# Kernel optimization log

Hardware: AMD Instinct MI355X
Metric: run time of the kernel (lower is better)

The kernel has to match this reference:

```python
import jax, jax.numpy as jnp
import numpy as np

DIM = 1024      # dim
FW = 14         # focal_window
FL = 2          # focal_level
FF = 4          # focal_factor


def _dwconv_gelu(x, w, b):
    # x: [B, C, S], w: [C, 1, k] depthwise kernel, torch 'same' padding
    k = w.shape[-1]
    y = jax.lax.conv_general_dilated(
        x, w, window_strides=(1,), padding=[((k - 1) // 2, k // 2)],
        feature_group_count=x.shape[1], dimension_numbers=('NCH', 'OIH', 'NCH'))
    return jax.nn.gelu(y + b[None, :, None], approximate=False)


def setup_inputs() -> dict:
    key = jax.random.key(0)
    ks = jax.random.split(key, 8)
    B, S, D = 8, 4096, DIM
    P = 2 * D + FL + 1  # 2051
    s = 0.02
    return {
        'input': jax.random.normal(ks[0], (B, S, D), jnp.float32),
        'W_in': jax.random.normal(ks[1], (D, P), jnp.float32) * s,
        'b_in': jnp.zeros((P,), jnp.float32),
        'w0': jax.random.normal(ks[2], (D, 1, FW), jnp.float32) * s,
        'b0': jnp.zeros((D,), jnp.float32),
        'w1': jax.random.normal(ks[3], (D, 1, FF + FW), jnp.float32) * s,  # kernel 18
        'b1': jnp.zeros((D,), jnp.float32),
        'W_ctx': jax.random.normal(ks[4], (D, D), jnp.float32) * s,
        'b_ctx': jnp.zeros((D,), jnp.float32),
        'W_out': jax.random.normal(ks[5], (D, D), jnp.float32) * s,
        'b_out': jnp.zeros((D,), jnp.float32),
    }


def reference(input, W_in, b_in, w0, b0, w1, b1, W_ctx, b_ctx, W_out, b_out):
    D = DIM
    # in_proj then permute to channel-first [B, 2D+FL+1, S]
    proj = (input @ W_in + b_in).transpose(0, 2, 1)
    query = proj[:, :D]            # [B, D, S]
    ctx = proj[:, D:2 * D]         # [B, D, S]
    gates = proj[:, 2 * D:]        # [B, FL+1, S]
    # hierarchical depthwise conv pyramid (context fed through successive levels)
    c0 = _dwconv_gelu(ctx, w0, b0)
    c1 = _dwconv_gelu(c0, w1, b1)
    context_all = c0 * gates[:, 0:1] + c1 * gates[:, 1:2]
    # global context branch
    g = jax.nn.gelu(c1.mean(axis=-1), approximate=False)  # [B, D]
    context_all = context_all + g[..., None] * gates[:, FL:FL + 1]
    # context_proj is a 1x1 conv == per-position linear over channels
    modulator = jnp.einsum('oc,bcs->bos', W_ctx, context_all) + b_ctx[None, :, None]
    out = (query * modulator).transpose(0, 2, 1)  # [B, S, D]
    return out @ W_out + b_out
```

## Files before the change

### kernel.cpp

```cpp
#include <hip/hip_runtime.h>

#define DIMC 1024
#define BATCH 8
#define SEQ 4096
#define BS (BATCH*SEQ)
#define PCOL 2051

typedef unsigned short ushort_t;
typedef __attribute__((ext_vector_type(8))) short short8;
typedef __attribute__((ext_vector_type(4))) float f32x4;
typedef __attribute__((ext_vector_type(4))) unsigned short us4;

__device__ __forceinline__ float bf2f(ushort_t u) {
    union { unsigned u32; float f; } v; v.u32 = ((unsigned)u) << 16; return v.f;
}
__device__ __forceinline__ ushort_t f2bf(float f) {
    union { float f; unsigned u; } v; v.f = f;
    unsigned r = v.u + 0x7fffu + ((v.u >> 16) & 1u);
    return (ushort_t)(r >> 16);
}
__device__ __forceinline__ float gelu_exact(float x) {
    return 0.5f * x * (1.0f + erff(x * 0.7071067811865475f));
}
__device__ __forceinline__ void gld16(const ushort_t* g, ushort_t* l) {
    __builtin_amdgcn_global_load_lds(
        (const __attribute__((address_space(1))) unsigned int*)g,
        (__attribute__((address_space(3))) unsigned int*)l, 16, 0, 0);
}

__global__ void cvt_f32_bf16(const float* __restrict__ src, ushort_t* __restrict__ dst, int n) {
    int i = (blockIdx.x * 256 + threadIdx.x) * 4;
    if (i >= n) return;
    f32x4 v = *(const f32x4*)(src + i);
    us4 o;
    #pragma unroll
    for (int j = 0; j < 4; j++) o[j] = f2bf(v[j]);
    *(us4*)(dst + i) = o;
}

__global__ void transpose_cvt(const float* __restrict__ src, ushort_t* __restrict__ dst,
                              int ld, int K) {
    __shared__ float tile[32][33];
    int tx = threadIdx.x & 31, ty = threadIdx.x >> 5;
    int n0 = blockIdx.x * 32, k0 = blockIdx.y * 32;
    #pragma unroll
    for (int j = 0; j < 4; j++)
        tile[ty + j * 8][tx] = src[(size_t)(k0 + ty + j * 8) * ld + n0 + tx];
    __syncthreads();
    #pragma unroll
    for (int j = 0; j < 4; j++)
        dst[(size_t)(n0 + ty + j * 8) * K + k0 + tx] = f2bf(tile[tx][ty + j * 8]);
}

__global__ void pack_gatesw(const float* __restrict__ W_in, float* __restrict__ wg) {
    int d = blockIdx.x * 256 + threadIdx.x;
    if (d >= 1024) return;
    const float* p = W_in + (size_t)d * PCOL + 2048;
    wg[d] = p[0]; wg[1024 + d] = p[1]; wg[2048 + d] = p[2];
}

__global__ void cvt_gates(const float* __restrict__ input, const float* __restrict__ wg,
                          const float* __restrict__ b_in, ushort_t* __restrict__ ibf,
                          float* __restrict__ gates) {
    int row = blockIdx.x, tid = threadIdx.x;
    int lane = tid & 63, wave = tid >> 6;
    size_t base = (size_t)row * 1024 + tid * 4;
    f32x4 v = *(const f32x4*)(input + base);
    us4 o;
    #pragma unroll
    for (int j = 0; j < 4; j++) o[j] = f2bf(v[j]);
    *(us4*)(ibf + base) = o;
    f32x4 w0v = *(const f32x4*)(wg + tid * 4);
    f32x4 w1v = *(const f32x4*)(wg + 1024 + tid * 4);
    f32x4 w2v = *(const f32x4*)(wg + 2048 + tid * 4);
    float a0 = 0, a1 = 0, a2 = 0;
    #pragma unroll
    for (int j = 0; j < 4; j++) { a0 += v[j] * w0v[j]; a1 += v[j] * w1v[j]; a2 += v[j] * w2v[j]; }
    #pragma unroll
    for (int off = 32; off; off >>= 1) {
        a0 += __shfl_down(a0, off, 64);
        a1 += __shfl_down(a1, off, 64);
        a2 += __shfl_down(a2, off, 64);
    }
    __shared__ float red[4][3];
    if (lane == 0) { red[wave][0] = a0; red[wave][1] = a1; red[wave][2] = a2; }
    __syncthreads();
    if (tid == 0) {
        gates[row * 4 + 0] = red[0][0] + red[1][0] + red[2][0] + red[3][0] + b_in[2048];
        gates[row * 4 + 1] = red[0][1] + red[1][1] + red[2][1] + red[3][1] + b_in[2049];
        gates[row * 4 + 2] = red[0][2] + red[1][2] + red[2][2] + red[3][2] + b_in[2050];
    }
}

template<int MODE>
__global__ __launch_bounds__(512, 2)
void gemm256(const ushort_t* __restrict__ A, const ushort_t* __restrict__ Bt,
             const float* __restrict__ bias, void* __restrict__ C,
             const ushort_t* __restrict__ Q, const float* __restrict__ gates,
             const float* __restrict__ vb, int K, int ldc, int ldq, int nbx, int tpb) {
    __shared__ ushort_t lA[2][16384];
    __shared__ ushort_t lB[2][16384];
    const int tid = threadIdx.x, lane = tid & 63, wave = tid >> 6;
    const int lr = lane & 15, kq = lane >> 4;
    const int wrm = wave >> 2, wrn = wave & 3;

    const int bid = blockIdx.x;
    const int chunk = (gridDim.x >> 3) * tpb;
    const int tile0 = (bid & 7) * chunk + (bid >> 3) * tpb;

    const int xsw = kq ^ (((lr >> 3) & 1) << 1);
    const int fBase = lr * 32 + xsw * 8;

    int srOff[2][2], ldsC[2][2];
    #pragma unroll
    for (int h = 0; h < 2; h++)
        #pragma unroll
        for (int j = 0; j < 2; j++) {
            int c = h * 1024 + j * 512 + tid;
            int sub = c >> 6, rl = (c >> 2) & 15, cc = c & 3;
            int r  = ((sub >> 1) << 4) | rl;
            int k8 = ((sub & 1) << 2) | (cc ^ (((rl >> 3) & 1) << 1));
            srOff[h][j] = r * K + k8 * 8;
            ldsC[h][j]  = (h * 1024 + j * 512 + (wave << 6)) << 3;
        }

    f32x4 acc[8][4];
    short8 af[2][2], bfr[4][2];

#define STG(ARR, bb, G, kt, h) do { \
    gld16((G) + (size_t)(kt) * 64 + srOff[h][0], &ARR[bb][ldsC[h][0]]); \
    gld16((G) + (size_t)(kt) * 64 + srOff[h][1], &ARR[bb][ldsC[h][1]]); \
} while (0)

#define PHASE(bb, qq, STAGE_STMT, DOVM) do { \
    if ((qq) == 0) { \
        _Pragma("unroll") \
        for (int nt = 0; nt < 4; nt++) { \
            bfr[nt][0] = *(const short8*)&lB[bb][fBase + ((wrn * 4 + nt) * 2 + 0) * 512]; \
            bfr[nt][1] = *(const short8*)&lB[bb][fBase + ((wrn * 4 + nt) * 2 + 1) * 512]; \
        } \
    } \
    af[0][0] = *(const short8*)&lA[bb][fBase + ((wrm * 8 + (qq) * 2 + 0) * 2 + 0) * 512]; \
    af[0][1] = *(const short8*)&lA[bb][fBase + ((wrm * 8 + (qq) * 2 + 0) * 2 + 1) * 512]; \
    af[1][0] = *(const short8*)&lA[bb][fBase + ((wrm * 8 + (qq) * 2 + 1) * 2 + 0) * 512]; \
    af[1][1] = *(const short8*)&lA[bb][fBase + ((wrm * 8 + (qq) * 2 + 1) * 2 + 1) * 512]; \
    STAGE_STMT; \
    __builtin_amdgcn_s_barrier(); \
    asm volatile("s_waitcnt lgkmcnt(0)" ::: "memory"); \
    __builtin_amdgcn_s_setprio(1); \
    _Pragma("unroll") \
    for (int mi = 0; mi < 2; mi++) \
        _Pragma("unroll") \
        for (int nt = 0; nt < 4; nt++) { \
            acc[(qq) * 2 + mi][nt] = __builtin_amdgcn_mfma_f32_16x16x32_bf16( \
                af[mi][0], bfr[nt][0], acc[(qq) * 2 + mi][nt], 0, 0, 0); \
            acc[(qq) * 2 + mi][nt] = __builtin_amdgcn_mfma_f32_16x16x32_bf16( \
                af[mi][1], bfr[nt][1], acc[(qq) * 2 + mi][nt], 0, 0, 0); \
        } \
    __builtin_amdgcn_s_setprio(0); \
    if (DOVM) asm volatile("s_waitcnt vmcnt(4)" ::: "memory"); \
    __builtin_amdgcn_s_barrier(); \
} while (0)

    const int KT = K >> 6;
    const int IT = K >> 7;

    int j = tile0;
    int bn = j % nbx, bm = j / nbx;
    const ushort_t* Ag = A + (size_t)bm * 256 * K;
    const ushort_t* Bg = Bt + (size_t)bn * 256 * K;

    STG(lA, 0, Ag, 0, 0); STG(lA, 0, Ag, 0, 1);
    STG(lB, 0, Bg, 0, 0); STG(lB, 0, Bg, 0, 1);
    STG(lB, 1, Bg, 1, 0); STG(lB, 1, Bg, 1, 1);
    asm volatile("s_waitcnt vmcnt(4)" ::: "memory");
    __builtin_amdgcn_s_barrier();

    for (int ti = 0; ti < tpb; ti++) {
        const int jn = (ti < tpb - 1) ? j + 1 : j;
        const int bnn = jn % nbx, bmn = jn / nbx;
        const ushort_t* Agn = A + (size_t)bmn * 256 * K;
        const ushort_t* Bgn = Bt + (size_t)bnn * 256 * K;

        #pragma unroll
        for (int i = 0; i < 8; i++)
            #pragma unroll
            for (int jj = 0; jj < 4; jj++)
                #pragma unroll
                for (int r = 0; r < 4; r++) acc[i][jj][r] = 0.f;

        for (int it = 0; it < IT - 1; it++) {
            const int t1 = 2 * it + 1, t2 = 2 * it + 2, t3 = 2 * it + 3;
            PHASE(0, 0, STG(lA, 1, Ag, t1, 0), 0);
            PHASE(0, 1, STG(lA, 1, Ag, t1, 1); STG(lB, 0, Bg, t2, 0), 0);
            PHASE(0, 2, STG(lB, 0, Bg, t2, 1), 0);
            PHASE(0, 3, (void)0, 1);
            PHASE(1, 0, STG(lA, 0, Ag, t2, 0), 0);
            PHASE(1, 1, STG(lA, 0, Ag, t2, 1); STG(lB, 1, Bg, t3, 0), 0);
            PHASE(1, 2, STG(lB, 1, Bg, t3, 1), 0);
            PHASE(1, 3, (void)0, 1);
        }
        PHASE(0, 0, STG(lA, 1, Ag, KT - 1, 0), 0);
        PHASE(0, 1, STG(lA, 1, Ag, KT - 1, 1); STG(lB, 0, Bgn, 0, 0), 0);
        PHASE(0, 2, STG(lB, 0, Bgn, 0, 1), 0);
        PHASE(0, 3, (void)0, 1);
        PHASE(1, 0, STG(lA, 0, Agn, 0, 0), 0);
        PHASE(1, 1, STG(lA, 0, Agn, 0, 1); STG(lB, 1, Bgn, 1, 0), 0);
        PHASE(1, 2, STG(lB, 1, Bgn, 1, 1), 0);
        PHASE(1, 3, (void)0, 1);

        const int bbatch = (bm * 256) >> 12;
        float biasv[4], vbv[4];
        #pragma unroll
        for (int nt = 0; nt < 4; nt++) {
            int col = bn * 256 + wrn * 64 + nt * 16 + lr;
            biasv[nt] = bias[col];
            if (MODE == 1) vbv[nt] = vb[bbatch * 1024 + col];
        }
        #pragma unroll
        for (int mt = 0; mt < 8; mt++) {
            #pragma unroll
            for (int r = 0; r < 4; r++) {
                int row = bm * 256 + wrm * 128 + mt * 16 + kq * 4 + r;
                size_t rowc = (size_t)row * ldc;
                float g2;
                if (MODE == 1) g2 = gates[row * 4 + 2];
                #pragma unroll
                for (int nt = 0; nt < 4; nt++) {
                    int col = bn * 256 + wrn * 64 + nt * 16 + lr;
                    float v = acc[mt][nt][r] + biasv[nt];
                    if (MODE == 1) {
                        v += g2 * vbv[nt];
                        v *= bf2f(Q[(size_t)row * ldq + col]);
                    }
                    if (MODE == 2) ((float*)C)[rowc + col] = v;
                    else           ((ushort_t*)C)[rowc + col] = f2bf(v);
                }
            }
        }

        j = jn; bm = bmn; bn = bnn; Ag = Agn; Bg = Bgn;
    }
#undef PHASE
#undef STG
    asm volatile("s_waitcnt vmcnt(0) lgkmcnt(0)" ::: "memory");
}

__global__ __launch_bounds__(256)
void dwconv_fused(const ushort_t* __restrict__ proj,
                  const float* __restrict__ w0, const float* __restrict__ b0,
                  const float* __restrict__ w1, const float* __restrict__ b1,
                  const float* __restrict__ gates,
                  ushort_t* __restrict__ P, float* __restrict__ G) {
    __shared__ float xc[94 * 64];
    __shared__ float x0[81 * 64];
    __shared__ float gl[2][64];
    __shared__ float rs[256];
    const int tid = threadIdx.x;
    const int s0 = blockIdx.x * 64, d0 = blockIdx.y * 64, b = blockIdx.z;
    for (int c = tid; c < 94 * 8; c += 256) {
        int r = c >> 3, dd = (c & 7) * 8;
        int s = s0 - 14 + r;
        float f[8];
        if (s >= 0 && s < SEQ) {
            short8 u = *(const short8*)&proj[(size_t)(b * SEQ + s) * 2048 + 1024 + d0 + dd];
            #pragma unroll
            for (int j = 0; j < 8; j++) f[j] = bf2f((ushort_t)u[j]);
        } else {
            #pragma unroll
            for (int j = 0; j < 8; j++) f[j] = 0.f;
        }
        f32x4 v0 = {f[0], f[1], f[2], f[3]}, v1 = {f[4], f[5], f[6], f[7]};
        *(f32x4*)&xc[r * 64 + dd] = v0;
        *(f32x4*)&xc[r * 64 + dd + 4] = v1;
    }
    if (tid < 64) gl[0][tid] = gates[(size_t)(b * SEQ + s0 + tid) * 4 + 0];
    else if (tid < 128) gl[1][tid - 64] = gates[(size_t)(b * SEQ + s0 + tid - 64) * 4 + 1];
    const int d = tid & 63, sc = tid >> 6;
    float wr0[14], wr1[18];
    #pragma unroll
    for (int t = 0; t < 14; t++) wr0[t] = w0[(size_t)(d0 + d) * 14 + t];
    float bb0 = b0[d0 + d];
    #pragma unroll
    for (int t = 0; t < 18; t++) wr1[t] = w1[(size_t)(d0 + d) * 18 + t];
    float bb1 = b1[d0 + d];
    __syncthreads();
    {
        float xw[34];
        int r0 = sc * 20;
        #pragma unroll
        for (int r = 0; r < 34; r++) xw[r] = xc[(r0 + r) * 64 + d];
        #pragma unroll
        for (int i = 0; i < 21; i++) {
            int rr = r0 + i;
            int s = s0 - 8 + rr;
            float acc = bb0;
            #pragma unroll
            for (int t = 0; t < 14; t++) acc += wr0[t] * xw[i + t];
            x0[rr * 64 + d] = (s >= 0 && s < SEQ) ? gelu_exact(acc) : 0.f;
        }
    }
    __syncthreads();
    float xw1[33];
    #pragma unroll
    for (int r = 0; r < 33; r++) xw1[r] = x0[(sc * 16 + r) * 64 + d];
    float psum = 0.f;
    #pragma unroll
    for (int i = 0; i < 16; i++) {
        float acc = bb1;
        #pragma unroll
        for (int t = 0; t < 18; t++) acc += wr1[t] * xw1[i + t];
        float c1 = gelu_exact(acc);
        psum += c1;
        float c0v = xw1[i + 8];
        int sl = sc * 16 + i;
        float pv = c0v * gl[0][sl] + c1 * gl[1][sl];
        P[(size_t)(b * SEQ + s0 + sl) * 1024 + d0 + d] = f2bf(pv);
    }
    rs[tid] = psum;
    __syncthreads();
    if (sc == 0)
        atomicAdd(&G[b * 1024 + d0 + d], rs[d] + rs[64 + d] + rs[128 + d] + rs[192 + d]);
}

__global__ __launch_bounds__(256)
void gemv_v(const float* __restrict__ G, const ushort_t* __restrict__ wctxB,
            float* __restrict__ v) {
    __shared__ float gg[1024];
    const int tid = threadIdx.x, b = blockIdx.y;
    for (int i = tid; i < 1024; i += 256)
        gg[i] = gelu_exact(G[b * 1024 + i] * (1.0f / (float)SEQ));
    __syncthreads();
    const int w = tid >> 6, lane = tid & 63;
    const int o = blockIdx.x * 4 + w;
    const ushort_t* wr = wctxB + (size_t)o * 1024;
    float acc = 0.f;
    #pragma unroll
    for (int j = 0; j < 16; j++)
        acc += gg[j * 64 + lane] * bf2f(wr[j * 64 + lane]);
    #pragma unroll
    for (int off = 32; off; off >>= 1) acc += __shfl_down(acc, off, 64);
    if (lane == 0) v[b * 1024 + o] = acc;
}

extern "C" void kernel_launch(void* const* d_in, const int* in_sizes, int n_in,
                              void* d_out, int out_size, void* d_ws, size_t ws_size,
                              hipStream_t stream) {
    const float* input = (const float*)d_in[0];
    const float* W_in  = (const float*)d_in[1];
    const float* b_in  = (const float*)d_in[2];
    const float* w0    = (const float*)d_in[3];
    const float* b0    = (const float*)d_in[4];
    const float* w1    = (const float*)d_in[5];
    const float* b1    = (const float*)d_in[6];
    const float* W_ctx = (const float*)d_in[7];
    const float* b_ctx = (const float*)d_in[8];
    const float* W_out = (const float*)d_in[9];
    const float* b_out = (const float*)d_in[10];

    char* ws = (char*)d_ws;
    size_t o = 0;
    ushort_t* ibf   = (ushort_t*)(ws + o); o += (size_t)BS * 1024 * 2;
    ushort_t* proj  = (ushort_t*)(ws + o); o += (size_t)BS * 2048 * 2;
    ushort_t* Y     = (ushort_t*)(ws + o); o += (size_t)BS * 1024 * 2;
    float*    gates = (float*)   (ws + o); o += (size_t)BS * 4 * 4;
    float*    G     = (float*)   (ws + o); o += (size_t)BATCH * 1024 * 4;
    float*    v     = (float*)   (ws + o); o += (size_t)BATCH * 1024 * 4;
    float*    wg    = (float*)   (ws + o); o += (size_t)3 * 1024 * 4;
    ushort_t* winT  = (ushort_t*)(ws + o); o += (size_t)2048 * 1024 * 2;
    ushort_t* wctxB = (ushort_t*)(ws + o); o += (size_t)1024 * 1024 * 2;
    ushort_t* woutT = (ushort_t*)(ws + o); o += (size_t)1024 * 1024 * 2;
    ushort_t* P = ibf;

    hipMemsetAsync(G, 0, BATCH * 1024 * sizeof(float), stream);
    pack_gatesw<<<4, 256, 0, stream>>>(W_in, wg);
    transpose_cvt<<<dim3(2048 / 32, 1024 / 32), 256, 0, stream>>>(W_in, winT, PCOL, 1024);
    cvt_f32_bf16<<<1024 * 1024 / 4 / 256, 256, 0, stream>>>(W_ctx, wctxB, 1024 * 1024);
    transpose_cvt<<<dim3(1024 / 32, 1024 / 32), 256, 0, stream>>>(W_out, woutT, 1024, 1024);
    cvt_gates<<<BS, 256, 0, stream>>>(input, wg, b_in, ibf, gates);
    gemm256<0><<<dim3(256), 512, 0, stream>>>(ibf, winT, b_in, proj,
        nullptr, nullptr, nullptr, 1024, 2048, 0, 8, 4);
    dwconv_fused<<<dim3(SEQ / 64, 16, BATCH), 256, 0, stream>>>(proj, w0, b0, w1, b1, gates, P, G);
    gemv_v<<<dim3(256, BATCH), 256, 0, stream>>>(G, wctxB, v);
    gemm256<1><<<dim3(256), 512, 0, stream>>>(P, wctxB, b_ctx, Y,
        proj, gates, v, 1024, 1024, 2048, 4, 2);
    gemm256<2><<<dim3(256), 512, 0, stream>>>(Y, woutT, b_out, d_out,
        nullptr, nullptr, nullptr, 1024, 1024, 0, 4, 2);
}
```

Baseline: 664.3 us.

## Merge GEMM k-loop phases from four to two per buffer

Restructures the GEMM main loop so each LDS buffer is consumed in two phases instead of four. Each phase loads fragments for two q-subtiles and issues twice as many MFMAs between barriers, which halves the barrier count per k-tile. Global-to-LDS staging is regrouped to match, and an extra lgkmcnt wait is added on the first half. The cost is higher register pressure from the doubled A-fragment set and a changed vmcnt wait cadence, which could reduce occupancy or change how loads overlap with compute.

```diff
diff --git a/kernel.cpp b/kernel.cpp
--- a/kernel.cpp
+++ b/kernel.cpp
@@ -125,38 +125,44 @@
         }
 
     f32x4 acc[8][4];
-    short8 af[2][2], bfr[4][2];
+    short8 af4[2][2][2], bfr[4][2];
 
 #define STG(ARR, bb, G, kt, h) do { \
     gld16((G) + (size_t)(kt) * 64 + srOff[h][0], &ARR[bb][ldsC[h][0]]); \
     gld16((G) + (size_t)(kt) * 64 + srOff[h][1], &ARR[bb][ldsC[h][1]]); \
 } while (0)
 
-#define PHASE(bb, qq, STAGE_STMT, DOVM) do { \
-    if ((qq) == 0) { \
+#define PHASE2(bb, half, STAGE_STMT, DOVM) do { \
+    if ((half) == 0) { \
         _Pragma("unroll") \
         for (int nt = 0; nt < 4; nt++) { \
             bfr[nt][0] = *(const short8*)&lB[bb][fBase + ((wrn * 4 + nt) * 2 + 0) * 512]; \
             bfr[nt][1] = *(const short8*)&lB[bb][fBase + ((wrn * 4 + nt) * 2 + 1) * 512]; \
         } \
     } \
-    af[0][0] = *(const short8*)&lA[bb][fBase + ((wrm * 8 + (qq) * 2 + 0) * 2 + 0) * 512]; \
-    af[0][1] = *(const short8*)&lA[bb][fBase + ((wrm * 8 + (qq) * 2 + 0) * 2 + 1) * 512]; \
-    af[1][0] = *(const short8*)&lA[bb][fBase + ((wrm * 8 + (qq) * 2 + 1) * 2 + 0) * 512]; \
-    af[1][1] = *(const short8*)&lA[bb][fBase + ((wrm * 8 + (qq) * 2 + 1) * 2 + 1) * 512]; \
+    _Pragma("unroll") \
+    for (int q = 0; q < 2; q++) \
+        _Pragma("unroll") \
+        for (int mi = 0; mi < 2; mi++) { \
+            af4[q][mi][0] = *(const short8*)&lA[bb][fBase + ((wrm * 8 + ((half) * 2 + q) * 2 + mi) * 2 + 0) * 512]; \
+            af4[q][mi][1] = *(const short8*)&lA[bb][fBase + ((wrm * 8 + ((half) * 2 + q) * 2 + mi) * 2 + 1) * 512]; \
+        } \
     STAGE_STMT; \
+    if ((half) == 0) asm volatile("s_waitcnt lgkmcnt(8)" ::: "memory"); \
     __builtin_amdgcn_s_barrier(); \
     asm volatile("s_waitcnt lgkmcnt(0)" ::: "memory"); \
     __builtin_amdgcn_s_setprio(1); \
     _Pragma("unroll") \
-    for (int mi = 0; mi < 2; mi++) \
+    for (int q = 0; q < 2; q++) \
         _Pragma("unroll") \
-        for (int nt = 0; nt < 4; nt++) { \
-            acc[(qq) * 2 + mi][nt] = __builtin_amdgcn_mfma_f32_16x16x32_bf16( \
-                af[mi][0], bfr[nt][0], acc[(qq) * 2 + mi][nt], 0, 0, 0); \
-            acc[(qq) * 2 + mi][nt] = __builtin_amdgcn_mfma_f32_16x16x32_bf16( \
-                af[mi][1], bfr[nt][1], acc[(qq) * 2 + mi][nt], 0, 0, 0); \
-        } \
+        for (int mi = 0; mi < 2; mi++) \
+            _Pragma("unroll") \
+            for (int nt = 0; nt < 4; nt++) { \
+                acc[((half) * 2 + q) * 2 + mi][nt] = __builtin_amdgcn_mfma_f32_16x16x32_bf16( \
+                    af4[q][mi][0], bfr[nt][0], acc[((half) * 2 + q) * 2 + mi][nt], 0, 0, 0); \
+                acc[((half) * 2 + q) * 2 + mi][nt] = __builtin_amdgcn_mfma_f32_16x16x32_bf16( \
+                    af4[q][mi][1], bfr[nt][1], acc[((half) * 2 + q) * 2 + mi][nt], 0, 0, 0); \
+            } \
     __builtin_amdgcn_s_setprio(0); \
     if (DOVM) asm volatile("s_waitcnt vmcnt(4)" ::: "memory"); \
     __builtin_amdgcn_s_barrier(); \
@@ -191,23 +197,15 @@
 
         for (int it = 0; it < IT - 1; it++) {
             const int t1 = 2 * it + 1, t2 = 2 * it + 2, t3 = 2 * it + 3;
-            PHASE(0, 0, STG(lA, 1, Ag, t1, 0), 0);
-            PHASE(0, 1, STG(lA, 1, Ag, t1, 1); STG(lB, 0, Bg, t2, 0), 0);
-            PHASE(0, 2, STG(lB, 0, Bg, t2, 1), 0);
-            PHASE(0, 3, (void)0, 1);
-            PHASE(1, 0, STG(lA, 0, Ag, t2, 0), 0);
-            PHASE(1, 1, STG(lA, 0, Ag, t2, 1); STG(lB, 1, Bg, t3, 0), 0);
-            PHASE(1, 2, STG(lB, 1, Bg, t3, 1), 0);
-            PHASE(1, 3, (void)0, 1);
-        }
-        PHASE(0, 0, STG(lA, 1, Ag, KT - 1, 0), 0);
-        PHASE(0, 1, STG(lA, 1, Ag, KT - 1, 1); STG(lB, 0, Bgn, 0, 0), 0);
-        PHASE(0, 2, STG(lB, 0, Bgn, 0, 1), 0);
-        PHASE(0, 3, (void)0, 1);
-        PHASE(1, 0, STG(lA, 0, Agn, 0, 0), 0);
-        PHASE(1, 1, STG(lA, 0, Agn, 0, 1); STG(lB, 1, Bgn, 1, 0), 0);
-        PHASE(1, 2, STG(lB, 1, Bgn, 1, 1), 0);
-        PHASE(1, 3, (void)0, 1);
+            PHASE2(0, 0, STG(lA, 1, Ag, t1, 0); STG(lA, 1, Ag, t1, 1), 0);
+            PHASE2(0, 1, STG(lB, 0, Bg, t2, 0); STG(lB, 0, Bg, t2, 1), 1);
+            PHASE2(1, 0, STG(lA, 0, Ag, t2, 0); STG(lA, 0, Ag, t2, 1), 0);
+            PHASE2(1, 1, STG(lB, 1, Bg, t3, 0); STG(lB, 1, Bg, t3, 1), 1);
+        }
+        PHASE2(0, 0, STG(lA, 1, Ag, KT - 1, 0); STG(lA, 1, Ag, KT - 1, 1), 0);
+        PHASE2(0, 1, STG(lB, 0, Bgn, 0, 0); STG(lB, 0, Bgn, 0, 1), 1);
+        PHASE2(1, 0, STG(lA, 0, Agn, 0, 0); STG(lA, 0, Agn, 0, 1), 0);
+        PHASE2(1, 1, STG(lB, 1, Bgn, 1, 0); STG(lB, 1, Bgn, 1, 1), 1);
 
         const int bbatch = (bm * 256) >> 12;
         float biasv[4], vbv[4];
@@ -241,7 +239,7 @@
 
         j = jn; bm = bmn; bn = bnn; Ag = Agn; Bg = Bgn;
     }
-#undef PHASE
+#undef PHASE2
 #undef STG
     asm volatile("s_waitcnt vmcnt(0) lgkmcnt(0)" ::: "memory");
 }
```

Result: no change. 662.7 us (-0.2%).
